# Optimization experiments

Hardware: AMD Instinct MI355X
Metric: run time of the kernel (lower is better)

Reference implementation:

```python
import jax, jax.numpy as jnp
import numpy as np

N = 50000      # nodes
E = 1600000    # edges (before self loops)
B = 512        # graphs
D = 128        # gcn dim (constant across the 3 GAT layers)
H = 1024       # hidden_dim
O = 128        # output_dim
NEG_SLOPE = 0.2


def setup_inputs() -> dict:
    key = jax.random.key(0)
    ks = jax.random.split(key, 24)
    inp = {
        "x": jax.random.normal(ks[0], (N, D), jnp.float32),
        "edge_index": jax.random.randint(ks[1], (2, E), 0, N, dtype=jnp.int64),
        "edge_weight": jax.random.uniform(ks[2], (E,), jnp.float32),
        "batch": jnp.sort(jax.random.randint(ks[3], (N,), 0, B, dtype=jnp.int64)),
    }
    s = 1.0 / np.sqrt(D)
    for i in range(3):
        k = 4 + 4 * i
        inp[f"W{i+1}"] = jax.random.normal(ks[k], (D, D), jnp.float32) * s
        inp[f"as{i+1}"] = jax.random.normal(ks[k + 1], (D,), jnp.float32) * s
        inp[f"ad{i+1}"] = jax.random.normal(ks[k + 2], (D,), jnp.float32) * s
        inp[f"b{i+1}"] = jnp.zeros((D,), jnp.float32)
    inp["Wf1"] = jax.random.normal(ks[16], (D, H), jnp.float32) * s
    inp["bf1"] = jnp.zeros((H,), jnp.float32)
    inp["Wf2"] = jax.random.normal(ks[17], (H, O), jnp.float32) * (1.0 / np.sqrt(H))
    inp["bf2"] = jnp.zeros((O,), jnp.float32)
    return inp


def gat_conv(x, src, dst, W, a_src, a_dst, b):
    """PyG GATConv, heads=1: gather -> leakyrelu -> segment softmax -> scatter-add."""
    h = x @ W                                   # [N, D]
    e = jax.nn.leaky_relu(jnp.take(h @ a_src, src) + jnp.take(h @ a_dst, dst), NEG_SLOPE)  # [E']
    m = jax.ops.segment_max(e, dst, num_segments=N)
    ex = jnp.exp(e - m[dst])
    denom = jax.ops.segment_sum(ex, dst, num_segments=N)
    alpha = ex / denom[dst]                      # segment softmax over incoming edges
    out = jax.ops.segment_sum(alpha[:, None] * h[src], dst, num_segments=N)
    return out + b


def reference(x, edge_index, edge_weight, batch,
              W1, as1, ad1, b1, W2, as2, ad2, b2, W3, as3, ad3, b3,
              Wf1, bf1, Wf2, bf2):
    # GATConv adds self loops; edge_weight is unused by GATConv (faithful to original)
    loop = jnp.arange(N, dtype=edge_index.dtype)
    src = jnp.concatenate([edge_index[0], loop])
    dst = jnp.concatenate([edge_index[1], loop])

    h = gat_conv(x, src, dst, W1, as1, ad1, b1)
    h = jax.nn.relu(gat_conv(h, src, dst, W2, as2, ad2, b2))
    h = jax.nn.relu(gat_conv(h, src, dst, W3, as3, ad3, b3))

    # global mean pool (gep)
    sums = jax.ops.segment_sum(h, batch, num_segments=B)        # [B, D]
    counts = jax.ops.segment_sum(jnp.ones((N,), h.dtype), batch, num_segments=B)
    pooled = sums / jnp.maximum(counts, 1.0)[:, None]

    # MLP head; dropout is identity at inference
    o = jax.nn.relu(pooled) @ Wf1 + bf1
    o = jax.nn.relu(o) @ Wf2 + bf2
    return o
```

## Files before the change

kernel.cpp:

```cpp
#include <hip/hip_runtime.h>
#include <cstdint>
#include <cstddef>

#define NEG_SLOPE 0.2f

typedef _Float16 f16x8 __attribute__((ext_vector_type(8)));
typedef float f32x4v __attribute__((ext_vector_type(4)));

__device__ __forceinline__ unsigned enc_f(float f) {
  unsigned u = __float_as_uint(f);
  return (u & 0x80000000u) ? ~u : (u | 0x80000000u);
}
__device__ __forceinline__ float dec_f(unsigned u) {
  return (u & 0x80000000u) ? __uint_as_float(u ^ 0x80000000u) : __uint_as_float(~u);
}
__device__ __forceinline__ unsigned short f2bf(float f) {
  unsigned u = __float_as_uint(f);
  unsigned r = u + 0x7fffu + ((u >> 16) & 1u);
  return (unsigned short)(r >> 16);
}
#define BLO(u) __uint_as_float((u) << 16)
#define BHI(u) __uint_as_float((u) & 0xffff0000u)

__global__ void k_init(int* counts, unsigned* maxPart, int N) {
  int n = blockIdx.x * blockDim.x + threadIdx.x;
  if (n < N) counts[n] = 1;
  if (n < 768) maxPart[n] = 0u;
}

__global__ void k_count_rank(const int* __restrict__ dst, int E,
                             int* counts, int* __restrict__ rank) {
  int i = (blockIdx.x * blockDim.x + threadIdx.x) * 4;
  if (i + 3 < E) {
    int4 d = *(const int4*)&dst[i];
    int4 r;
    r.x = atomicAdd(&counts[d.x], 1);
    r.y = atomicAdd(&counts[d.y], 1);
    r.z = atomicAdd(&counts[d.z], 1);
    r.w = atomicAdd(&counts[d.w], 1);
    *(int4*)&rank[i] = r;
  } else {
    for (int e = i; e < E; e++) rank[e] = atomicAdd(&counts[dst[e]], 1);
  }
}
__global__ void k_count_rank_s(const int* __restrict__ dst, int E,
                               int* counts, int* __restrict__ rank) {
  int e = blockIdx.x * blockDim.x + threadIdx.x;
  if (e < E) rank[e] = atomicAdd(&counts[dst[e]], 1);
}

__global__ __launch_bounds__(1024) void k_scan1(const int* __restrict__ counts, int N,
                                                int* __restrict__ row_ptr, int* __restrict__ part) {
  __shared__ int tmp[1024];
  int t = threadIdx.x;
  int i = blockIdx.x * 1024 + t;
  int v = (i < N) ? counts[i] : 0;
  tmp[t] = v;
  __syncthreads();
  for (int off = 1; off < 1024; off <<= 1) {
    int u = (t >= off) ? tmp[t - off] : 0;
    __syncthreads();
    tmp[t] += u;
    __syncthreads();
  }
  if (i < N) row_ptr[i + 1] = tmp[t];
  if (t == 1023) part[blockIdx.x] = tmp[t];
}

__global__ void k_scan2(int* part, int nb, int* row_ptr) {
  if (threadIdx.x == 0 && blockIdx.x == 0) {
    int run = 0;
    for (int b = 0; b < nb; b++) { int v = part[b]; part[b] = run; run += v; }
    row_ptr[0] = 0;
  }
}

__global__ __launch_bounds__(1024) void k_scan3(int* __restrict__ row_ptr,
                                                const int* __restrict__ part, int N) {
  int i = blockIdx.x * 1024 + threadIdx.x;
  if (i < N) row_ptr[i + 1] += part[blockIdx.x];
}

__global__ void k_fill_self(const int* __restrict__ row_ptr, int* __restrict__ col, int N) {
  int n = blockIdx.x * blockDim.x + threadIdx.x;
  if (n < N) col[row_ptr[n]] = n;
}

__global__ void k_fill(const int* __restrict__ src, const int* __restrict__ dst,
                       const int* __restrict__ rank, int E,
                       const int* __restrict__ row_ptr, int* __restrict__ col) {
  int i = (blockIdx.x * blockDim.x + threadIdx.x) * 4;
  if (i + 3 < E) {
    int4 s = *(const int4*)&src[i];
    int4 d = *(const int4*)&dst[i];
    int4 r = *(const int4*)&rank[i];
    col[row_ptr[d.x] + r.x] = s.x;
    col[row_ptr[d.y] + r.y] = s.y;
    col[row_ptr[d.z] + r.z] = s.z;
    col[row_ptr[d.w] + r.w] = s.w;
  } else {
    for (int e = i; e < E; e++) col[row_ptr[dst[e]] + rank[e]] = src[e];
  }
}
__global__ void k_fill_s(const int* __restrict__ src, const int* __restrict__ dst,
                         const int* __restrict__ rank, int E,
                         const int* __restrict__ row_ptr, int* __restrict__ col) {
  int e = blockIdx.x * blockDim.x + threadIdx.x;
  if (e < E) col[row_ptr[dst[e]] + rank[e]] = src[e];
}

#define AST 136
#define WST 136
#define HST 132
__global__ __launch_bounds__(256) void k_gemm_fused(const float* __restrict__ A,
                                                    const float* __restrict__ W,
                                                    unsigned short* __restrict__ hb,
                                                    const float* __restrict__ asrc,
                                                    const float* __restrict__ adst,
                                                    float* __restrict__ sv, float* __restrict__ dv,
                                                    unsigned* __restrict__ maxSlot, int M) {
  __shared__ __align__(16) char smem[64 * AST * 2 + 128 * WST * 2];
  _Float16* Ah = (_Float16*)smem;
  _Float16* Wt = (_Float16*)(smem + 64 * AST * 2);
  float*    hS = (float*)(smem + 64 * AST * 2);
  __shared__ float redmax[4];
  int t = threadIdx.x;
  int rowbase = blockIdx.x * 64;

  for (int i = t; i < 64 * 32; i += 256) {
    int r = i >> 5, c4 = (i & 31) << 2;
    int gr = rowbase + r;
    float4 v = make_float4(0.f, 0.f, 0.f, 0.f);
    if (gr < M) v = *(const float4*)&A[(size_t)gr * 128 + c4];
    _Float16 tmp[4] = {(_Float16)v.x, (_Float16)v.y, (_Float16)v.z, (_Float16)v.w};
    *(short4*)&Ah[r * AST + c4] = *(short4*)tmp;
  }
  for (int i = t; i < 128 * 32; i += 256) {
    int r = i >> 5, c4 = (i & 31) << 2;
    float4 v = *(const float4*)&W[(size_t)r * 128 + c4];
    Wt[(c4 + 0) * WST + r] = (_Float16)v.x;
    Wt[(c4 + 1) * WST + r] = (_Float16)v.y;
    Wt[(c4 + 2) * WST + r] = (_Float16)v.z;
    Wt[(c4 + 3) * WST + r] = (_Float16)v.w;
  }
  __syncthreads();

  int wave = t >> 6, lane = t & 63, quad = lane >> 4, l15 = lane & 15;
  f32x4v acc[4][2];
#pragma unroll
  for (int mt = 0; mt < 4; mt++)
#pragma unroll
    for (int nt = 0; nt < 2; nt++) {
      acc[mt][nt][0] = 0.f; acc[mt][nt][1] = 0.f; acc[mt][nt][2] = 0.f; acc[mt][nt][3] = 0.f;
    }

#pragma unroll
  for (int s = 0; s < 4; s++) {
    int k0 = (s << 5) + (quad << 3);
    f16x8 af[4], bf[2];
#pragma unroll
    for (int mt = 0; mt < 4; mt++)
      af[mt] = *(f16x8*)&Ah[(mt * 16 + l15) * AST + k0];
#pragma unroll
    for (int nt = 0; nt < 2; nt++)
      bf[nt] = *(f16x8*)&Wt[(wave * 32 + nt * 16 + l15) * WST + k0];
#pragma unroll
    for (int mt = 0; mt < 4; mt++)
#pragma unroll
      for (int nt = 0; nt < 2; nt++)
        acc[mt][nt] = __builtin_amdgcn_mfma_f32_16x16x32_f16(af[mt], bf[nt], acc[mt][nt], 0, 0, 0);
  }
  __syncthreads();

#pragma unroll
  for (int mt = 0; mt < 4; mt++)
#pragma unroll
    for (int nt = 0; nt < 2; nt++)
#pragma unroll
      for (int rr = 0; rr < 4; rr++)
        hS[(mt * 16 + quad * 4 + rr) * HST + wave * 32 + nt * 16 + l15] = acc[mt][nt][rr];
  __syncthreads();

  int tx = t & 31, ty = t >> 5;
  float4 av  = *(const float4*)&asrc[tx * 4];
  float4 adv = *(const float4*)&adst[tx * 4];
  float wmax = -1e30f;
#pragma unroll
  for (int r8 = 0; r8 < 8; r8++) {
    int row = r8 * 8 + ty;
    int gr = rowbase + row;
    float4 hv = *(float4*)&hS[row * HST + tx * 4];
    float ps = hv.x * av.x + hv.y * av.y + hv.z * av.z + hv.w * av.w;
    float pd = hv.x * adv.x + hv.y * adv.y + hv.z * adv.z + hv.w * adv.w;
#pragma unroll
    for (int mask = 16; mask; mask >>= 1) {
      ps += __shfl_xor(ps, mask);
      pd += __shfl_xor(pd, mask);
    }
    if (gr < M) {
      ushort4 hq;
      hq.x = f2bf(hv.x); hq.y = f2bf(hv.y); hq.z = f2bf(hv.z); hq.w = f2bf(hv.w);
      *(ushort4*)&hb[(size_t)gr * 128 + tx * 4] = hq;
      if (tx == 0) { sv[gr] = ps; dv[gr] = pd; wmax = fmaxf(wmax, ps); }
    }
  }
#pragma unroll
  for (int mask = 32; mask; mask >>= 1) wmax = fmaxf(wmax, __shfl_xor(wmax, mask));
  if ((t & 63) == 0) redmax[t >> 6] = wmax;
  __syncthreads();
  if (t == 0) {
    float mx = fmaxf(fmaxf(redmax[0], redmax[1]), fmaxf(redmax[2], redmax[3]));
    atomicMax(&maxSlot[blockIdx.x & 255], enc_f(mx));
  }
}

__global__ __launch_bounds__(256) void k_agg(const unsigned short* __restrict__ hb,
                                             const float* __restrict__ sv,
                                             const float* __restrict__ dv,
                                             const int* __restrict__ row_ptr,
                                             const int* __restrict__ col,
                                             const float* __restrict__ bias,
                                             const unsigned* __restrict__ maxSlot,
                                             float* __restrict__ out, int N, int relu) {
  int wid = (int)((blockIdx.x * (size_t)blockDim.x + threadIdx.x) >> 6);
  int lane = threadIdx.x & 63;
  if (wid >= N) return;

  unsigned mp = max(max(maxSlot[lane], maxSlot[lane + 64]),
                    max(maxSlot[lane + 128], maxSlot[lane + 192]));
#pragma unroll
  for (int off = 32; off; off >>= 1) mp = max(mp, __shfl_xor(mp, off));
  float maxS = dec_f(mp);

  int beg = row_ptr[wid], end = row_ptr[wid + 1];
  float dn = dv[wid];
  float m = maxS + dn;
  m = (m > 0.f) ? m : NEG_SLOPE * m;

  int g = lane >> 4, sub = lane & 15;
  const uint32_t* hbu = (const uint32_t*)hb;
  float acc[8];
#pragma unroll
  for (int k = 0; k < 8; k++) acc[k] = 0.f;
  float dsum = 0.f;

  for (int j = beg + g; j < end; j += 4) {
    int sn = col[j];
    float e = sv[sn] + dn;
    e = (e > 0.f) ? e : NEG_SLOPE * e;
    float wgt = __expf(e - m);
    dsum += wgt;
    uint4 hv = *(const uint4*)(hbu + (size_t)sn * 64 + sub * 4);
    acc[0] += wgt * BLO(hv.x); acc[1] += wgt * BHI(hv.x);
    acc[2] += wgt * BLO(hv.y); acc[3] += wgt * BHI(hv.y);
    acc[4] += wgt * BLO(hv.z); acc[5] += wgt * BHI(hv.z);
    acc[6] += wgt * BLO(hv.w); acc[7] += wgt * BHI(hv.w);
  }
  dsum += __shfl_xor(dsum, 16);
  dsum += __shfl_xor(dsum, 32);
#pragma unroll
  for (int k = 0; k < 8; k++) {
    acc[k] += __shfl_xor(acc[k], 16);
    acc[k] += __shfl_xor(acc[k], 32);
  }
  if (lane < 16) {
    float inv = 1.f / dsum;
    float4 b0 = *(const float4*)&bias[sub * 8];
    float4 b1 = *(const float4*)&bias[sub * 8 + 4];
    float4 o0, o1;
    o0.x = acc[0] * inv + b0.x; o0.y = acc[1] * inv + b0.y;
    o0.z = acc[2] * inv + b0.z; o0.w = acc[3] * inv + b0.w;
    o1.x = acc[4] * inv + b1.x; o1.y = acc[5] * inv + b1.y;
    o1.z = acc[6] * inv + b1.z; o1.w = acc[7] * inv + b1.w;
    if (relu) {
      o0.x = fmaxf(o0.x, 0.f); o0.y = fmaxf(o0.y, 0.f); o0.z = fmaxf(o0.z, 0.f); o0.w = fmaxf(o0.w, 0.f);
      o1.x = fmaxf(o1.x, 0.f); o1.y = fmaxf(o1.y, 0.f); o1.z = fmaxf(o1.z, 0.f); o1.w = fmaxf(o1.w, 0.f);
    }
    float* op = &out[(size_t)wid * 128 + sub * 8];
    *(float4*)op = o0;
    *(float4*)(op + 4) = o1;
  }
}

__global__ void k_bounds(const int* __restrict__ batch, int N, int B, int* __restrict__ gstart) {
  int n = blockIdx.x * blockDim.x + threadIdx.x;
  if (n >= N) return;
  int cur = batch[n];
  if (n == 0) {
    for (int g = 0; g <= cur; g++) gstart[g] = 0;
  } else {
    int prev = batch[n - 1];
    for (int g = prev + 1; g <= cur; g++) gstart[g] = n;
  }
  if (n == N - 1) {
    for (int g = cur + 1; g <= B; g++) gstart[g] = N;
  }
}

__global__ __launch_bounds__(128) void k_pool(const float* __restrict__ h,
                                              const int* __restrict__ gstart,
                                              float* __restrict__ pooled, int B) {
  int b = blockIdx.x, c = threadIdx.x;
  int s0 = gstart[b], s1 = gstart[b + 1];
  float acc = 0.f;
  for (int n = s0; n < s1; n++) acc += h[(size_t)n * 128 + c];
  int cnt = s1 - s0;
  float p = acc / (float)(cnt > 0 ? cnt : 1);
  pooled[b * 128 + c] = fmaxf(p, 0.f);
}

__global__ __launch_bounds__(256) void k_mlp(const float* __restrict__ pooled,
                                             const float* __restrict__ Wf1,
                                             const float* __restrict__ bf1,
                                             const float* __restrict__ Wf2,
                                             const float* __restrict__ bf2,
                                             float* __restrict__ out, int B) {
  __shared__ float P[4][128];
  __shared__ float H1[4][1024];
  __shared__ float R[4][128];
  int t = threadIdx.x;
  int g0 = blockIdx.x * 4;

  for (int i = t; i < 4 * 128; i += 256) {
    int gi = i >> 7, c = i & 127;
    P[gi][c] = (g0 + gi < B) ? pooled[(size_t)(g0 + gi) * 128 + c] : 0.f;
  }
  __syncthreads();

#pragma unroll
  for (int cb = 0; cb < 4; cb++) {
    int c = cb * 256 + t;
    float a0 = 0.f, a1 = 0.f, a2 = 0.f, a3 = 0.f;
    for (int k = 0; k < 128; k++) {
      float w = Wf1[(size_t)k * 1024 + c];
      a0 += P[0][k] * w; a1 += P[1][k] * w; a2 += P[2][k] * w; a3 += P[3][k] * w;
    }
    float b = bf1[c];
    H1[0][c] = fmaxf(a0 + b, 0.f);
    H1[1][c] = fmaxf(a1 + b, 0.f);
    H1[2][c] = fmaxf(a2 + b, 0.f);
    H1[3][c] = fmaxf(a3 + b, 0.f);
  }
  __syncthreads();

  int c = t & 127, hh = t >> 7;
  float a0 = 0.f, a1 = 0.f, a2 = 0.f, a3 = 0.f;
  int k0 = hh * 512;
  for (int k = k0; k < k0 + 512; k++) {
    float w = Wf2[(size_t)k * 128 + c];
    a0 += H1[0][k] * w; a1 += H1[1][k] * w; a2 += H1[2][k] * w; a3 += H1[3][k] * w;
  }
  if (hh == 1) { R[0][c] = a0; R[1][c] = a1; R[2][c] = a2; R[3][c] = a3; }
  __syncthreads();
  if (hh == 0) {
    float b = bf2[c];
    float o0 = a0 + R[0][c] + b;
    float o1 = a1 + R[1][c] + b;
    float o2 = a2 + R[2][c] + b;
    float o3 = a3 + R[3][c] + b;
    if (g0 + 0 < B) out[(size_t)(g0 + 0) * 128 + c] = o0;
    if (g0 + 1 < B) out[(size_t)(g0 + 1) * 128 + c] = o1;
    if (g0 + 2 < B) out[(size_t)(g0 + 2) * 128 + c] = o2;
    if (g0 + 3 < B) out[(size_t)(g0 + 3) * 128 + c] = o3;
  }
}

extern "C" void kernel_launch(void* const* d_in, const int* in_sizes, int n_in,
                              void* d_out, int out_size, void* d_ws, size_t ws_size,
                              hipStream_t stream) {
  const float* x     = (const float*)d_in[0];
  const int*   ei    = (const int*)d_in[1];
  const int*   batch = (const int*)d_in[3];
  const float* W1 = (const float*)d_in[4];
  const float* as1 = (const float*)d_in[5];
  const float* ad1 = (const float*)d_in[6];
  const float* b1 = (const float*)d_in[7];
  const float* W2 = (const float*)d_in[8];
  const float* as2 = (const float*)d_in[9];
  const float* ad2 = (const float*)d_in[10];
  const float* b2 = (const float*)d_in[11];
  const float* W3 = (const float*)d_in[12];
  const float* as3 = (const float*)d_in[13];
  const float* ad3 = (const float*)d_in[14];
  const float* b3 = (const float*)d_in[15];
  const float* Wf1 = (const float*)d_in[16];
  const float* bf1 = (const float*)d_in[17];
  const float* Wf2 = (const float*)d_in[18];
  const float* bf2 = (const float*)d_in[19];

  const int N = in_sizes[0] / 128;
  const int E = in_sizes[1] / 2;
  const int B = out_size / 128;

  char* base = (char*)d_ws;
  size_t off = 0;
  auto carve = [&](size_t bytes) -> void* {
    off = (off + 255) & ~(size_t)255;
    void* p = base + off;
    off += bytes;
    return p;
  };
  int* counts   = (int*)carve((size_t)N * 4);
  int* row_ptr  = (int*)carve((size_t)(N + 1) * 4);
  int* rank     = (int*)carve((size_t)E * 4);
  int* col      = (int*)carve((size_t)(E + N) * 4);
  int* part     = (int*)carve(1024 * 4);
  int* gstart   = (int*)carve((size_t)(B + 1) * 4);
  unsigned* maxPart = (unsigned*)carve(768 * 4);
  float* sbuf   = (float*)carve((size_t)N * 4);
  float* dbuf   = (float*)carve((size_t)N * 4);
  unsigned short* hb = (unsigned short*)carve((size_t)N * 128 * 2);
  float* abuf   = (float*)carve((size_t)N * 128 * 4);
  float* pooled = (float*)carve((size_t)B * 128 * 4);

  const int* srcp = ei;
  const int* dstp = ei + E;
  const int nb = (N + 1023) / 1024;

  hipLaunchKernelGGL(k_init, dim3((N + 255) / 256), dim3(256), 0, stream, counts, maxPart, N);
  if ((E & 3) == 0) {
    int nq = E / 4;
    hipLaunchKernelGGL(k_count_rank, dim3((nq + 255) / 256), dim3(256), 0, stream, dstp, E, counts, rank);
  } else {
    hipLaunchKernelGGL(k_count_rank_s, dim3((E + 255) / 256), dim3(256), 0, stream, dstp, E, counts, rank);
  }
  hipLaunchKernelGGL(k_scan1, dim3(nb), dim3(1024), 0, stream, counts, N, row_ptr, part);
  hipLaunchKernelGGL(k_scan2, dim3(1), dim3(64), 0, stream, part, nb, row_ptr);
  hipLaunchKernelGGL(k_scan3, dim3(nb), dim3(1024), 0, stream, row_ptr, part, N);
  hipLaunchKernelGGL(k_fill_self, dim3((N + 255) / 256), dim3(256), 0, stream, row_ptr, col, N);
  if ((E & 3) == 0) {
    int nq = E / 4;
    hipLaunchKernelGGL(k_fill, dim3((nq + 255) / 256), dim3(256), 0, stream, srcp, dstp, rank, E, row_ptr, col);
  } else {
    hipLaunchKernelGGL(k_fill_s, dim3((E + 255) / 256), dim3(256), 0, stream, srcp, dstp, rank, E, row_ptr, col);
  }
  hipLaunchKernelGGL(k_bounds, dim3((N + 255) / 256), dim3(256), 0, stream, batch, N, B, gstart);

  const float* Wl[3] = {W1, W2, W3};
  const float* al[3] = {as1, as2, as3};
  const float* dl[3] = {ad1, ad2, ad3};
  const float* bl[3] = {b1, b2, b3};
  const float* cur = x;
  for (int L = 0; L < 3; L++) {
    hipLaunchKernelGGL(k_gemm_fused, dim3((N + 63) / 64), dim3(256), 0, stream,
                       cur, Wl[L], hb, al[L], dl[L], sbuf, dbuf, maxPart + L * 256, N);
    hipLaunchKernelGGL(k_agg, dim3((N + 3) / 4), dim3(256), 0, stream,
                       hb, sbuf, dbuf, row_ptr, col, bl[L], maxPart + L * 256, abuf, N, (L > 0) ? 1 : 0);
    cur = abuf;
  }

  hipLaunchKernelGGL(k_pool, dim3(B), dim3(128), 0, stream, abuf, gstart, pooled, B);
  hipLaunchKernelGGL(k_mlp, dim3((B + 3) / 4), dim3(256), 0, stream,
                     pooled, Wf1, bf1, Wf2, bf2, (float*)d_out, B);
}
```

Before: 580.6 us.

## Rebuild CSR via shared-memory range histograms and store activations in fp16

```diff
diff --git a/kernel.cpp b/kernel.cpp
--- a/kernel.cpp
+++ b/kernel.cpp
@@ -3,6 +3,8 @@
 #include <cstddef>
 
 #define NEG_SLOPE 0.2f
+#define RNG 6250
+#define NCHUNK 32
 
 typedef _Float16 f16x8 __attribute__((ext_vector_type(8)));
 typedef float f32x4v __attribute__((ext_vector_type(4)));
@@ -14,47 +16,58 @@
 __device__ __forceinline__ float dec_f(unsigned u) {
   return (u & 0x80000000u) ? __uint_as_float(u ^ 0x80000000u) : __uint_as_float(~u);
 }
-__device__ __forceinline__ unsigned short f2bf(float f) {
-  unsigned u = __float_as_uint(f);
-  unsigned r = u + 0x7fffu + ((u >> 16) & 1u);
-  return (unsigned short)(r >> 16);
-}
-#define BLO(u) __uint_as_float((u) << 16)
-#define BHI(u) __uint_as_float((u) & 0xffff0000u)
-
-__global__ void k_init(int* counts, unsigned* maxPart, int N) {
+
+#define AST 136
+#define WST 136
+#define HST 132
+#define SMEM_BYTES (64 * AST * 2 + 128 * WST * 2)
+
+__global__ void k_bounds(const int* __restrict__ batch, int N, int B,
+                         int* __restrict__ gstart, unsigned* __restrict__ maxPart) {
   int n = blockIdx.x * blockDim.x + threadIdx.x;
-  if (n < N) counts[n] = 1;
   if (n < 768) maxPart[n] = 0u;
-}
-
-__global__ void k_count_rank(const int* __restrict__ dst, int E,
-                             int* counts, int* __restrict__ rank) {
-  int i = (blockIdx.x * blockDim.x + threadIdx.x) * 4;
-  if (i + 3 < E) {
-    int4 d = *(const int4*)&dst[i];
-    int4 r;
-    r.x = atomicAdd(&counts[d.x], 1);
-    r.y = atomicAdd(&counts[d.y], 1);
-    r.z = atomicAdd(&counts[d.z], 1);
-    r.w = atomicAdd(&counts[d.w], 1);
-    *(int4*)&rank[i] = r;
+  if (n >= N) return;
+  int cur = batch[n];
+  if (n == 0) {
+    for (int g = 0; g <= cur; g++) gstart[g] = 0;
   } else {
-    for (int e = i; e < E; e++) rank[e] = atomicAdd(&counts[dst[e]], 1);
-  }
-}
-__global__ void k_count_rank_s(const int* __restrict__ dst, int E,
-                               int* counts, int* __restrict__ rank) {
-  int e = blockIdx.x * blockDim.x + threadIdx.x;
-  if (e < E) rank[e] = atomicAdd(&counts[dst[e]], 1);
-}
-
-__global__ __launch_bounds__(1024) void k_scan1(const int* __restrict__ counts, int N,
+    int prev = batch[n - 1];
+    for (int g = prev + 1; g <= cur; g++) gstart[g] = n;
+  }
+  if (n == N - 1) {
+    for (int g = cur + 1; g <= B; g++) gstart[g] = N;
+  }
+}
+
+__global__ __launch_bounds__(256) void k_hist(const int* __restrict__ dst, int E, int chunkE,
+                                              int* __restrict__ c, int N) {
+  __shared__ int h[RNG];
+  int ri = blockIdx.x, ci = blockIdx.y;
+  int r0 = ri * RNG;
+  int rn = min(RNG, N - r0);
+  for (int i = threadIdx.x; i < rn; i += 256) h[i] = 0;
+  __syncthreads();
+  int e0 = ci * chunkE, e1 = min(e0 + chunkE, E);
+  for (int e = e0 + threadIdx.x; e < e1; e += 256) {
+    int d = dst[e] - r0;
+    if ((unsigned)d < (unsigned)rn) atomicAdd(&h[d], 1);
+  }
+  __syncthreads();
+  int* cp = c + (size_t)ci * N + r0;
+  for (int i = threadIdx.x; i < rn; i += 256) cp[i] = h[i];
+}
+
+__global__ __launch_bounds__(1024) void k_scan1(const int* __restrict__ c, int N,
                                                 int* __restrict__ row_ptr, int* __restrict__ part) {
   __shared__ int tmp[1024];
   int t = threadIdx.x;
   int i = blockIdx.x * 1024 + t;
-  int v = (i < N) ? counts[i] : 0;
+  int v = 0;
+  if (i < N) {
+    v = 1;
+#pragma unroll
+    for (int p = 0; p < NCHUNK; p++) v += c[(size_t)p * N + i];
+  }
   tmp[t] = v;
   __syncthreads();
   for (int off = 1; off < 1024; off <<= 1) {
@@ -67,73 +80,89 @@
   if (t == 1023) part[blockIdx.x] = tmp[t];
 }
 
-__global__ void k_scan2(int* part, int nb, int* row_ptr) {
-  if (threadIdx.x == 0 && blockIdx.x == 0) {
-    int run = 0;
-    for (int b = 0; b < nb; b++) { int v = part[b]; part[b] = run; run += v; }
-    row_ptr[0] = 0;
-  }
-}
-
 __global__ __launch_bounds__(1024) void k_scan3(int* __restrict__ row_ptr,
                                                 const int* __restrict__ part, int N) {
-  int i = blockIdx.x * 1024 + threadIdx.x;
-  if (i < N) row_ptr[i + 1] += part[blockIdx.x];
-}
-
-__global__ void k_fill_self(const int* __restrict__ row_ptr, int* __restrict__ col, int N) {
+  __shared__ int s_off;
+  int bi = blockIdx.x;
+  if (threadIdx.x == 0) {
+    int run = 0;
+    for (int b = 0; b < bi; b++) run += part[b];
+    s_off = run;
+    if (bi == 0) row_ptr[0] = 0;
+  }
+  __syncthreads();
+  int i = bi * 1024 + threadIdx.x;
+  if (i < N) row_ptr[i + 1] += s_off;
+}
+
+__global__ void k_base(const int* __restrict__ row_ptr, const int* __restrict__ c,
+                       int* __restrict__ base, int* __restrict__ col, int N) {
   int n = blockIdx.x * blockDim.x + threadIdx.x;
-  if (n < N) col[row_ptr[n]] = n;
-}
-
-__global__ void k_fill(const int* __restrict__ src, const int* __restrict__ dst,
-                       const int* __restrict__ rank, int E,
-                       const int* __restrict__ row_ptr, int* __restrict__ col) {
-  int i = (blockIdx.x * blockDim.x + threadIdx.x) * 4;
-  if (i + 3 < E) {
-    int4 s = *(const int4*)&src[i];
-    int4 d = *(const int4*)&dst[i];
-    int4 r = *(const int4*)&rank[i];
-    col[row_ptr[d.x] + r.x] = s.x;
-    col[row_ptr[d.y] + r.y] = s.y;
-    col[row_ptr[d.z] + r.z] = s.z;
-    col[row_ptr[d.w] + r.w] = s.w;
-  } else {
-    for (int e = i; e < E; e++) col[row_ptr[dst[e]] + rank[e]] = src[e];
-  }
-}
-__global__ void k_fill_s(const int* __restrict__ src, const int* __restrict__ dst,
-                         const int* __restrict__ rank, int E,
-                         const int* __restrict__ row_ptr, int* __restrict__ col) {
-  int e = blockIdx.x * blockDim.x + threadIdx.x;
-  if (e < E) col[row_ptr[dst[e]] + rank[e]] = src[e];
-}
-
-#define AST 136
-#define WST 136
-#define HST 132
-__global__ __launch_bounds__(256) void k_gemm_fused(const float* __restrict__ A,
+  if (n >= N) return;
+  int b = row_ptr[n];
+  col[b] = n;
+  b++;
+#pragma unroll
+  for (int ci = 0; ci < NCHUNK; ci++) {
+    base[(size_t)ci * N + n] = b;
+    b += c[(size_t)ci * N + n];
+  }
+}
+
+__global__ __launch_bounds__(256) void k_place(const int* __restrict__ src,
+                                               const int* __restrict__ dst, int E, int chunkE,
+                                               const int* __restrict__ base,
+                                               int* __restrict__ col, int N) {
+  __shared__ int h[RNG];
+  int ri = blockIdx.x, ci = blockIdx.y;
+  int r0 = ri * RNG;
+  int rn = min(RNG, N - r0);
+  const int* bp = base + (size_t)ci * N + r0;
+  for (int i = threadIdx.x; i < rn; i += 256) h[i] = bp[i];
+  __syncthreads();
+  int e0 = ci * chunkE, e1 = min(e0 + chunkE, E);
+  for (int e = e0 + threadIdx.x; e < e1; e += 256) {
+    int d = dst[e] - r0;
+    if ((unsigned)d < (unsigned)rn) {
+      int p = atomicAdd(&h[d], 1);
+      col[p] = src[e];
+    }
+  }
+}
+
+__global__ __launch_bounds__(256) void k_gemm_fused(const float* __restrict__ A32,
+                                                    const unsigned short* __restrict__ A16,
                                                     const float* __restrict__ W,
                                                     unsigned short* __restrict__ hb,
                                                     const float* __restrict__ asrc,
                                                     const float* __restrict__ adst,
                                                     float* __restrict__ sv, float* __restrict__ dv,
                                                     unsigned* __restrict__ maxSlot, int M) {
-  __shared__ __align__(16) char smem[64 * AST * 2 + 128 * WST * 2];
+  __shared__ __align__(16) char smem[SMEM_BYTES];
+  __shared__ float redmax[4];
   _Float16* Ah = (_Float16*)smem;
   _Float16* Wt = (_Float16*)(smem + 64 * AST * 2);
   float*    hS = (float*)(smem + 64 * AST * 2);
-  __shared__ float redmax[4];
   int t = threadIdx.x;
   int rowbase = blockIdx.x * 64;
 
-  for (int i = t; i < 64 * 32; i += 256) {
-    int r = i >> 5, c4 = (i & 31) << 2;
-    int gr = rowbase + r;
-    float4 v = make_float4(0.f, 0.f, 0.f, 0.f);
-    if (gr < M) v = *(const float4*)&A[(size_t)gr * 128 + c4];
-    _Float16 tmp[4] = {(_Float16)v.x, (_Float16)v.y, (_Float16)v.z, (_Float16)v.w};
-    *(short4*)&Ah[r * AST + c4] = *(short4*)tmp;
+  if (A16) {
+    for (int i = t; i < 64 * 16; i += 256) {
+      int r = i >> 4, c8 = (i & 15) << 3;
+      int gr = rowbase + r;
+      uint4 v = make_uint4(0u, 0u, 0u, 0u);
+      if (gr < M) v = *(const uint4*)&A16[(size_t)gr * 128 + c8];
+      *(uint4*)&Ah[r * AST + c8] = v;
+    }
+  } else {
+    for (int i = t; i < 64 * 32; i += 256) {
+      int r = i >> 5, c4 = (i & 31) << 2;
+      int gr = rowbase + r;
+      float4 v = make_float4(0.f, 0.f, 0.f, 0.f);
+      if (gr < M) v = *(const float4*)&A32[(size_t)gr * 128 + c4];
+      _Float16 tmp[4] = {(_Float16)v.x, (_Float16)v.y, (_Float16)v.z, (_Float16)v.w};
+      *(short4*)&Ah[r * AST + c4] = *(short4*)tmp;
+    }
   }
   for (int i = t; i < 128 * 32; i += 256) {
     int r = i >> 5, c4 = (i & 31) << 2;
@@ -198,9 +227,8 @@
       pd += __shfl_xor(pd, mask);
     }
     if (gr < M) {
-      ushort4 hq;
-      hq.x = f2bf(hv.x); hq.y = f2bf(hv.y); hq.z = f2bf(hv.z); hq.w = f2bf(hv.w);
-      *(ushort4*)&hb[(size_t)gr * 128 + tx * 4] = hq;
+      _Float16 hq[4] = {(_Float16)hv.x, (_Float16)hv.y, (_Float16)hv.z, (_Float16)hv.w};
+      *(uint2*)&hb[(size_t)gr * 128 + tx * 4] = *(uint2*)hq;
       if (tx == 0) { sv[gr] = ps; dv[gr] = pd; wmax = fmaxf(wmax, ps); }
     }
   }
@@ -221,7 +249,8 @@
                                              const int* __restrict__ col,
                                              const float* __restrict__ bias,
                                              const unsigned* __restrict__ maxSlot,
-                                             float* __restrict__ out, int N, int relu) {
+                                             unsigned short* __restrict__ out16,
+                                             int N, int relu) {
   int wid = (int)((blockIdx.x * (size_t)blockDim.x + threadIdx.x) >> 6);
   int lane = threadIdx.x & 63;
   if (wid >= N) return;
@@ -244,18 +273,37 @@
   for (int k = 0; k < 8; k++) acc[k] = 0.f;
   float dsum = 0.f;
 
-  for (int j = beg + g; j < end; j += 4) {
+  int j = beg + g;
+  float wc = 0.f;
+  uint4 hc = make_uint4(0u, 0u, 0u, 0u);
+  if (j < end) {
     int sn = col[j];
     float e = sv[sn] + dn;
     e = (e > 0.f) ? e : NEG_SLOPE * e;
-    float wgt = __expf(e - m);
-    dsum += wgt;
-    uint4 hv = *(const uint4*)(hbu + (size_t)sn * 64 + sub * 4);
-    acc[0] += wgt * BLO(hv.x); acc[1] += wgt * BHI(hv.x);
-    acc[2] += wgt * BLO(hv.y); acc[3] += wgt * BHI(hv.y);
-    acc[4] += wgt * BLO(hv.z); acc[5] += wgt * BHI(hv.z);
-    acc[6] += wgt * BLO(hv.w); acc[7] += wgt * BHI(hv.w);
-  }
+    wc = __expf(e - m);
+    hc = *(const uint4*)(hbu + (size_t)sn * 64 + sub * 4);
+  }
+  j += 4;
+  while (j < end) {
+    int sn = col[j];
+    float e = sv[sn] + dn;
+    e = (e > 0.f) ? e : NEG_SLOPE * e;
+    float wn = __expf(e - m);
+    uint4 hn = *(const uint4*)(hbu + (size_t)sn * 64 + sub * 4);
+    dsum += wc;
+    const _Float16* hp = (const _Float16*)&hc;
+#pragma unroll
+    for (int k = 0; k < 8; k++) acc[k] += wc * (float)hp[k];
+    wc = wn; hc = hn;
+    j += 4;
+  }
+  {
+    dsum += wc;
+    const _Float16* hp = (const _Float16*)&hc;
+#pragma unroll
+    for (int k = 0; k < 8; k++) acc[k] += wc * (float)hp[k];
+  }
+
   dsum += __shfl_xor(dsum, 16);
   dsum += __shfl_xor(dsum, 32);
 #pragma unroll
@@ -265,48 +313,37 @@
   }
   if (lane < 16) {
     float inv = 1.f / dsum;
-    float4 b0 = *(const float4*)&bias[sub * 8];
-    float4 b1 = *(const float4*)&bias[sub * 8 + 4];
-    float4 o0, o1;
-    o0.x = acc[0] * inv + b0.x; o0.y = acc[1] * inv + b0.y;
-    o0.z = acc[2] * inv + b0.z; o0.w = acc[3] * inv + b0.w;
-    o1.x = acc[4] * inv + b1.x; o1.y = acc[5] * inv + b1.y;
-    o1.z = acc[6] * inv + b1.z; o1.w = acc[7] * inv + b1.w;
-    if (relu) {
-      o0.x = fmaxf(o0.x, 0.f); o0.y = fmaxf(o0.y, 0.f); o0.z = fmaxf(o0.z, 0.f); o0.w = fmaxf(o0.w, 0.f);
-      o1.x = fmaxf(o1.x, 0.f); o1.y = fmaxf(o1.y, 0.f); o1.z = fmaxf(o1.z, 0.f); o1.w = fmaxf(o1.w, 0.f);
-    }
-    float* op = &out[(size_t)wid * 128 + sub * 8];
-    *(float4*)op = o0;
-    *(float4*)(op + 4) = o1;
-  }
-}
-
-__global__ void k_bounds(const int* __restrict__ batch, int N, int B, int* __restrict__ gstart) {
-  int n = blockIdx.x * blockDim.x + threadIdx.x;
-  if (n >= N) return;
-  int cur = batch[n];
-  if (n == 0) {
-    for (int g = 0; g <= cur; g++) gstart[g] = 0;
-  } else {
-    int prev = batch[n - 1];
-    for (int g = prev + 1; g <= cur; g++) gstart[g] = n;
-  }
-  if (n == N - 1) {
-    for (int g = cur + 1; g <= B; g++) gstart[g] = N;
-  }
-}
-
-__global__ __launch_bounds__(128) void k_pool(const float* __restrict__ h,
-                                              const int* __restrict__ gstart,
-                                              float* __restrict__ pooled, int B) {
+    float o[8];
+    const float* bp = &bias[sub * 8];
+#pragma unroll
+    for (int k = 0; k < 8; k++) {
+      o[k] = acc[k] * inv + bp[k];
+      if (relu) o[k] = fmaxf(o[k], 0.f);
+    }
+    _Float16 q[8];
+#pragma unroll
+    for (int k = 0; k < 8; k++) q[k] = (_Float16)o[k];
+    *(uint4*)&out16[(size_t)wid * 128 + sub * 8] = *(uint4*)q;
+  }
+}
+
+__global__ __launch_bounds__(64) void k_pool(const unsigned short* __restrict__ h16,
+                                             const int* __restrict__ gstart,
+                                             float* __restrict__ pooled, int B) {
   int b = blockIdx.x, c = threadIdx.x;
   int s0 = gstart[b], s1 = gstart[b + 1];
-  float acc = 0.f;
-  for (int n = s0; n < s1; n++) acc += h[(size_t)n * 128 + c];
+  const uint32_t* hu = (const uint32_t*)h16;
+  float a0 = 0.f, a1 = 0.f;
+  for (int n = s0; n < s1; n++) {
+    union { uint32_t u; _Float16 h[2]; } cv;
+    cv.u = hu[(size_t)n * 64 + c];
+    a0 += (float)cv.h[0];
+    a1 += (float)cv.h[1];
+  }
   int cnt = s1 - s0;
-  float p = acc / (float)(cnt > 0 ? cnt : 1);
-  pooled[b * 128 + c] = fmaxf(p, 0.f);
+  float inv = 1.f / (float)(cnt > 0 ? cnt : 1);
+  pooled[b * 128 + 2 * c]     = fmaxf(a0 * inv, 0.f);
+  pooled[b * 128 + 2 * c + 1] = fmaxf(a1 * inv, 0.f);
 }
 
 __global__ __launch_bounds__(256) void k_mlp(const float* __restrict__ pooled,
@@ -392,64 +429,64 @@
   const int E = in_sizes[1] / 2;
   const int B = out_size / 128;
 
-  char* base = (char*)d_ws;
+  char* base_ws = (char*)d_ws;
   size_t off = 0;
   auto carve = [&](size_t bytes) -> void* {
     off = (off + 255) & ~(size_t)255;
-    void* p = base + off;
+    void* p = base_ws + off;
     off += bytes;
     return p;
   };
-  int* counts   = (int*)carve((size_t)N * 4);
+  int* c        = (int*)carve((size_t)NCHUNK * N * 4);
+  int* base     = (int*)carve((size_t)NCHUNK * N * 4);
   int* row_ptr  = (int*)carve((size_t)(N + 1) * 4);
-  int* rank     = (int*)carve((size_t)E * 4);
   int* col      = (int*)carve((size_t)(E + N) * 4);
   int* part     = (int*)carve(1024 * 4);
   int* gstart   = (int*)carve((size_t)(B + 1) * 4);
   unsigned* maxPart = (unsigned*)carve(768 * 4);
   float* sbuf   = (float*)carve((size_t)N * 4);
   float* dbuf   = (float*)carve((size_t)N * 4);
-  unsigned short* hb = (unsigned short*)carve((size_t)N * 128 * 2);
-  float* abuf   = (float*)carve((size_t)N * 128 * 4);
+  unsigned short* hb  = (unsigned short*)carve((size_t)N * 128 * 2);
+  unsigned short* a16 = (unsigned short*)carve((size_t)N * 128 * 2);
   float* pooled = (float*)carve((size_t)B * 128 * 4);
 
   const int* srcp = ei;
   const int* dstp = ei + E;
   const int nb = (N + 1023) / 1024;
-
-  hipLaunchKernelGGL(k_init, dim3((N + 255) / 256), dim3(256), 0, stream, counts, maxPart, N);
-  if ((E & 3) == 0) {
-    int nq = E / 4;
-    hipLaunchKernelGGL(k_count_rank, dim3((nq + 255) / 256), dim3(256), 0, stream, dstp, E, counts, rank);
-  } else {
-    hipLaunchKernelGGL(k_count_rank_s, dim3((E + 255) / 256), dim3(256), 0, stream, dstp, E, counts, rank);
-  }
-  hipLaunchKernelGGL(k_scan1, dim3(nb), dim3(1024), 0, stream, counts, N, row_ptr, part);
-  hipLaunchKernelGGL(k_scan2, dim3(1), dim3(64), 0, stream, part, nb, row_ptr);
+  const int R = (N + RNG - 1) / RNG;
+  const int chunkE = (E + NCHUNK - 1) / NCHUNK;
+  const int Gg = (N + 63) / 64;
+
+  hipLaunchKernelGGL(k_bounds, dim3((N + 255) / 256), dim3(256), 0, stream,
+                     batch, N, B, gstart, maxPart);
+
+  hipLaunchKernelGGL(k_gemm_fused, dim3(Gg), dim3(256), 0, stream,
+                     x, (const unsigned short*)nullptr, W1, hb, as1, ad1,
+                     sbuf, dbuf, maxPart + 0 * 256, N);
+
+  hipLaunchKernelGGL(k_hist, dim3(R, NCHUNK), dim3(256), 0, stream, dstp, E, chunkE, c, N);
+  hipLaunchKernelGGL(k_scan1, dim3(nb), dim3(1024), 0, stream, c, N, row_ptr, part);
   hipLaunchKernelGGL(k_scan3, dim3(nb), dim3(1024), 0, stream, row_ptr, part, N);
-  hipLaunchKernelGGL(k_fill_self, dim3((N + 255) / 256), dim3(256), 0, stream, row_ptr, col, N);
-  if ((E & 3) == 0) {
-    int nq = E / 4;
-    hipLaunchKernelGGL(k_fill, dim3((nq + 255) / 256), dim3(256), 0, stream, srcp, dstp, rank, E, row_ptr, col);
-  } else {
-    hipLaunchKernelGGL(k_fill_s, dim3((E + 255) / 256), dim3(256), 0, stream, srcp, dstp, rank, E, row_ptr, col);
-  }
-  hipLaunchKernelGGL(k_bounds, dim3((N + 255) / 256), dim3(256), 0, stream, batch, N, B, gstart);
-
-  const float* Wl[3] = {W1, W2, W3};
-  const float* al[3] = {as1, as2, as3};
-  const float* dl[3] = {ad1, ad2, ad3};
-  const float* bl[3] = {b1, b2, b3};
-  const float* cur = x;
-  for (int L = 0; L < 3; L++) {
-    hipLaunchKernelGGL(k_gemm_fused, dim3((N + 63) / 64), dim3(256), 0, stream,
-                       cur, Wl[L], hb, al[L], dl[L], sbuf, dbuf, maxPart + L * 256, N);
-    hipLaunchKernelGGL(k_agg, dim3((N + 3) / 4), dim3(256), 0, stream,
-                       hb, sbuf, dbuf, row_ptr, col, bl[L], maxPart + L * 256, abuf, N, (L > 0) ? 1 : 0);
-    cur = abuf;
-  }
-
-  hipLaunchKernelGGL(k_pool, dim3(B), dim3(128), 0, stream, abuf, gstart, pooled, B);
+  hipLaunchKernelGGL(k_base, dim3((N + 255) / 256), dim3(256), 0, stream, row_ptr, c, base, col, N);
+  hipLaunchKernelGGL(k_place, dim3(R, NCHUNK), dim3(256), 0, stream,
+                     srcp, dstp, E, chunkE, base, col, N);
+
+  hipLaunchKernelGGL(k_agg, dim3((N + 3) / 4), dim3(256), 0, stream,
+                     hb, sbuf, dbuf, row_ptr, col, b1, maxPart + 0 * 256, a16, N, 0);
+
+  hipLaunchKernelGGL(k_gemm_fused, dim3(Gg), dim3(256), 0, stream,
+                     (const float*)nullptr, a16, W2, hb, as2, ad2,
+                     sbuf, dbuf, maxPart + 1 * 256, N);
+  hipLaunchKernelGGL(k_agg, dim3((N + 3) / 4), dim3(256), 0, stream,
+                     hb, sbuf, dbuf, row_ptr, col, b2, maxPart + 1 * 256, a16, N, 1);
+
+  hipLaunchKernelGGL(k_gemm_fused, dim3(Gg), dim3(256), 0, stream,
+                     (const float*)nullptr, a16, W3, hb, as3, ad3,
+                     sbuf, dbuf, maxPart + 2 * 256, N);
+  hipLaunchKernelGGL(k_agg, dim3((N + 3) / 4), dim3(256), 0, stream,
+                     hb, sbuf, dbuf, row_ptr, col, b3, maxPart + 2 * 256, a16, N, 1);
+
+  hipLaunchKernelGGL(k_pool, dim3(B), dim3(64), 0, stream, a16, gstart, pooled, B);
   hipLaunchKernelGGL(k_mlp, dim3((B + 3) / 4), dim3(256), 0, stream,
                      pooled, Wf1, bf1, Wf2, bf2, (float*)d_out, B);
 }
```

New measurement: 665.9 us. +14.7%, slower.
